# Performance work log

Hardware: AMD Instinct MI355X
Metric: run time of the kernel (lower is better)

The kernel has to match this reference:

```python
import jax, jax.numpy as jnp
import numpy as np

T, S, B, E, H = 1024, 1024, 4, 1024, 16
D = E // H
SCALE = D ** -0.5


def setup_inputs() -> dict:
    key = jax.random.key(0)
    ks = jax.random.split(key, 10)
    std = 0.02
    return {
        "q": jax.random.normal(ks[0], (T, B, E), jnp.float32),
        "k": jax.random.normal(ks[1], (S, B, E), jnp.float32),
        "v": jax.random.normal(ks[2], (S, B, E), jnp.float32),
        "Wq": jax.random.normal(ks[3], (E, E), jnp.float32) * std,
        "Wk": jax.random.normal(ks[4], (E, E), jnp.float32) * std,
        "Wv": jax.random.normal(ks[5], (E, E), jnp.float32) * std,
        "Wp": jax.random.normal(ks[6], (E, E), jnp.float32) * std,
        "bp": jnp.zeros((E,), jnp.float32),
        "attn_bias": jax.random.normal(ks[7], (B, H, T, S), jnp.float32) * std,
        "key_padding_mask": jax.random.bernoulli(ks[8], 0.1, (B, S)),
    }


def reference(q, k, v, Wq, Wk, Wv, Wp, bp, attn_bias, key_padding_mask):
    # projections (no bias: qkv_bias=False); torch Linear is x @ W.T
    qh = (q @ Wq.T).reshape(T, B, H, D).transpose(1, 2, 0, 3) * SCALE  # [B,H,T,D]
    kh = (k @ Wk.T).reshape(S, B, H, D).transpose(1, 2, 0, 3)          # [B,H,S,D]
    vh = (v @ Wv.T).reshape(S, B, H, D).transpose(1, 2, 0, 3)          # [B,H,S,D]

    scores = jnp.einsum("bhid,bhjd->bhij", qh, kh) + attn_bias        # [B,H,T,S]
    # detached max-subtract (as in original)
    scores = scores - jax.lax.stop_gradient(scores.max(axis=-1, keepdims=True))

    mask = key_padding_mask[:, None, None, :]                          # [B,1,1,S], True = masked
    neg = jnp.finfo(scores.dtype).min
    attn = jax.nn.softmax(jnp.where(mask, neg, scores), axis=-1)
    attn = jnp.where(mask, jnp.zeros((), scores.dtype), attn)          # XSoftmax: zero masked probs

    out = jnp.einsum("bhij,bhjd->bhid", attn, vh)                      # [B,H,T,D]
    out = out.transpose(2, 0, 1, 3).reshape(T, B, E)                   # [T,B,E]
    out = out @ Wp.T + bp                                              # output projection
    return (out, attn)
```

## Files before the change

kernel.cpp:

```cpp
#include <hip/hip_runtime.h>
#include <math.h>

constexpr int T_ = 1024, S_ = 1024, B_ = 4, E_ = 1024, H_ = 16, D_ = 64;
constexpr float SCALE_ = 0.125f;
constexpr size_t NH_ = (size_t)B_ * H_ * T_ * D_;
constexpr size_t EE_ = (size_t)E_ * E_;

typedef _Float16 h8 __attribute__((ext_vector_type(8)));
typedef _Float16 h4 __attribute__((ext_vector_type(4)));
typedef float f4 __attribute__((ext_vector_type(4)));

__device__ inline f4 mfma16(h8 a, h8 b, f4 c) {
    return __builtin_amdgcn_mfma_f32_16x16x32_f16(a, b, c, 0, 0, 0);
}

__device__ inline void gload_lds16(const void* g, void* l) {
    __builtin_amdgcn_global_load_lds(
        (const __attribute__((address_space(1))) void*)g,
        (__attribute__((address_space(3))) void*)l, 16, 0, 0);
}

__global__ __launch_bounds__(256) void cvt_all(
    const float* __restrict__ q, const float* __restrict__ k,
    const float* __restrict__ v, const float* __restrict__ wq,
    const float* __restrict__ wk, const float* __restrict__ wv,
    const float* __restrict__ wp, _Float16* __restrict__ dst)
{
    const int i8 = blockIdx.x * 256 + threadIdx.x;
    constexpr int BIG = (int)(NH_ / 8);
    constexpr int WSZ = (int)(EE_ / 8);
    const float* src;
    int loc;
    if (i8 < 3 * BIG) {
        int t = i8 / BIG; loc = i8 - t * BIG;
        src = t == 0 ? q : (t == 1 ? k : v);
    } else {
        int r = i8 - 3 * BIG;
        int t = r / WSZ; loc = r - t * WSZ;
        src = t == 0 ? wq : (t == 1 ? wk : (t == 2 ? wv : wp));
    }
    const float* p = src + (size_t)loc * 8;
    float4 a = *(const float4*)p;
    float4 b = *(const float4*)(p + 4);
    h8 o;
    o[0] = (_Float16)a.x; o[1] = (_Float16)a.y;
    o[2] = (_Float16)a.z; o[3] = (_Float16)a.w;
    o[4] = (_Float16)b.x; o[5] = (_Float16)b.y;
    o[6] = (_Float16)b.z; o[7] = (_Float16)b.w;
    *(h8*)&dst[(size_t)i8 * 8] = o;
}

template <typename EPI>
__device__ inline void gemm_core(
    const _Float16* __restrict__ A, const _Float16* __restrict__ W,
    int m0, int n0, EPI epi)
{
    __shared__ _Float16 As[64][64];
    __shared__ _Float16 Bs[128][64];

    const int tid = threadIdx.x;
    const int w = tid >> 6, l = tid & 63, lr = l & 15, lg = l >> 4;
    const int wr = w >> 2, wc = w & 3;

    const int srow = (w << 3) + (l >> 3);
    const int sg   = (l & 7) ^ (srow & 7);
    char* AsB = (char*)As;
    char* BsB = (char*)Bs;
    char* ldsA  = AsB + w * 1024;
    char* ldsB0 = BsB + w * 1024;
    char* ldsB1 = BsB + 8192 + w * 1024;

    f4 acc[2][2];
#pragma unroll
    for (int mi = 0; mi < 2; ++mi)
#pragma unroll
        for (int ni = 0; ni < 2; ++ni) acc[mi][ni] = (f4){0.f, 0.f, 0.f, 0.f};

    for (int k0 = 0; k0 < 1024; k0 += 64) {
        gload_lds16(&A[(size_t)(m0 + srow) * 1024 + k0 + sg * 8], ldsA);
        gload_lds16(&W[(size_t)(n0 + srow) * 1024 + k0 + sg * 8], ldsB0);
        gload_lds16(&W[(size_t)(n0 + 64 + srow) * 1024 + k0 + sg * 8], ldsB1);
        __syncthreads();
#pragma unroll
        for (int kk = 0; kk < 2; ++kk) {
            h8 af[2], bf[2];
#pragma unroll
            for (int mi = 0; mi < 2; ++mi) {
                int r = wr * 32 + mi * 16 + lr, kc = kk * 4 + lg;
                af[mi] = *(const h8*)(AsB + r * 128 + ((kc ^ (r & 7)) << 4));
            }
#pragma unroll
            for (int ni = 0; ni < 2; ++ni) {
                int r = wc * 32 + ni * 16 + lr, kc = kk * 4 + lg;
                bf[ni] = *(const h8*)(BsB + r * 128 + ((kc ^ (r & 7)) << 4));
            }
#pragma unroll
            for (int mi = 0; mi < 2; ++mi)
#pragma unroll
                for (int ni = 0; ni < 2; ++ni)
                    acc[mi][ni] = mfma16(af[mi], bf[ni], acc[mi][ni]);
        }
        __syncthreads();
    }

#pragma unroll
    for (int mi = 0; mi < 2; ++mi)
#pragma unroll
        for (int ni = 0; ni < 2; ++ni)
#pragma unroll
            for (int r = 0; r < 4; ++r) {
                int row = m0 + wr * 32 + mi * 16 + lg * 4 + r;
                int col = n0 + wc * 32 + ni * 16 + lr;
                epi(row, col, acc[mi][ni][r]);
            }
}

template <typename EPI>
__device__ inline void gemm_core128(
    const _Float16* __restrict__ A, const _Float16* __restrict__ W,
    int m0, int n0, EPI epi)
{
    __shared__ _Float16 As[128][64];
    __shared__ _Float16 Bs[128][64];

    const int tid = threadIdx.x;
    const int w = tid >> 6, l = tid & 63, lr = l & 15, lg = l >> 4;
    const int wr = w >> 2, wc = w & 3;

    char* AsB = (char*)As;
    char* BsB = (char*)Bs;

    f4 acc[4][2];
#pragma unroll
    for (int mi = 0; mi < 4; ++mi)
#pragma unroll
        for (int ni = 0; ni < 2; ++ni) acc[mi][ni] = (f4){0.f, 0.f, 0.f, 0.f};

    for (int k0 = 0; k0 < 1024; k0 += 64) {
#pragma unroll
        for (int d = 0; d < 2; ++d) {
            int row = w * 16 + d * 8 + (l >> 3);
            int sg = (l & 7) ^ (row & 7);
            gload_lds16(&A[(size_t)(m0 + row) * 1024 + k0 + sg * 8],
                        AsB + (w * 16 + d * 8) * 128);
            gload_lds16(&W[(size_t)(n0 + row) * 1024 + k0 + sg * 8],
                        BsB + (w * 16 + d * 8) * 128);
        }
        __syncthreads();
#pragma unroll
        for (int kk = 0; kk < 2; ++kk) {
            h8 af[4], bf[2];
#pragma unroll
            for (int mi = 0; mi < 4; ++mi) {
                int r = wr * 64 + mi * 16 + lr, kc = kk * 4 + lg;
                af[mi] = *(const h8*)(AsB + r * 128 + ((kc ^ (r & 7)) << 4));
            }
#pragma unroll
            for (int ni = 0; ni < 2; ++ni) {
                int r = wc * 32 + ni * 16 + lr, kc = kk * 4 + lg;
                bf[ni] = *(const h8*)(BsB + r * 128 + ((kc ^ (r & 7)) << 4));
            }
#pragma unroll
            for (int mi = 0; mi < 4; ++mi)
#pragma unroll
                for (int ni = 0; ni < 2; ++ni)
                    acc[mi][ni] = mfma16(af[mi], bf[ni], acc[mi][ni]);
        }
        __syncthreads();
    }

#pragma unroll
    for (int mi = 0; mi < 4; ++mi)
#pragma unroll
        for (int ni = 0; ni < 2; ++ni)
#pragma unroll
            for (int r = 0; r < 4; ++r) {
                int row = m0 + wr * 64 + mi * 16 + lg * 4 + r;
                int col = n0 + wc * 32 + ni * 16 + lr;
                epi(row, col, acc[mi][ni][r]);
            }
}

__global__ __launch_bounds__(512) void qkv_gemm(
    const _Float16* __restrict__ q16, const _Float16* __restrict__ k16,
    const _Float16* __restrict__ v16, const _Float16* __restrict__ Wq16,
    const _Float16* __restrict__ Wk16, const _Float16* __restrict__ Wv16,
    _Float16* __restrict__ qh, _Float16* __restrict__ kh,
    _Float16* __restrict__ vhT)
{
    const int z = blockIdx.z;
    const _Float16* A = z == 0 ? q16 : (z == 1 ? k16 : v16);
    const _Float16* W = z == 0 ? Wq16 : (z == 1 ? Wk16 : Wv16);
    _Float16* C = z == 0 ? qh : (z == 1 ? kh : vhT);
    const float scale = (z == 0) ? SCALE_ : 1.0f;
    const int m0 = blockIdx.x * 128, n0 = blockIdx.y * 128;

    if (z < 2) {
        gemm_core128(A, W, m0, n0, [&](int row, int col, float vv) {
            int t = row >> 2, b = row & 3, h = col >> 6, d = col & 63;
            C[(((size_t)b * H_ + h) * T_ + t) * D_ + d] = (_Float16)(vv * scale);
        });
    } else {
        gemm_core128(A, W, m0, n0, [&](int row, int col, float vv) {
            int s = row >> 2, b = row & 3, h = col >> 6, d = col & 63;
            C[(((size_t)b * H_ + h) * D_ + d) * S_ + s] = (_Float16)vv;
        });
    }
}

__global__ __launch_bounds__(512) void out_gemm(
    const _Float16* __restrict__ oh, const _Float16* __restrict__ Wp16,
    const float* __restrict__ bp, float* __restrict__ out)
{
    const int m0 = blockIdx.x * 64, n0 = blockIdx.y * 128;
    gemm_core(oh, Wp16, m0, n0, [&](int row, int col, float vv) {
        out[(size_t)row * E_ + col] = vv + bp[col];
    });
}

__global__ __launch_bounds__(512, 6) void fused_attn(
    const _Float16* __restrict__ qh, const _Float16* __restrict__ kh,
    const _Float16* __restrict__ vhT, const float* __restrict__ bias,
    const int* __restrict__ mask, float* __restrict__ attn,
    _Float16* __restrict__ oh)
{
    __shared__ _Float16 Pf[16 * 1024];
    __shared__ int aux_i[1024];
    __shared__ float wsum[8][16];
    __shared__ float sinv16[16];
    char* Pb = (char*)Pf;

    const int bid = blockIdx.x;
    const int vid = (bid & 7) * 512 + (bid >> 3);
    const int bh = vid >> 6;
    const int t0 = (vid & 63) * 16;
    const int b = bh >> 4, h = bh & 15;
    const int tid = threadIdx.x;
    const int w = tid >> 6, l = tid & 63, lr = l & 15, lg = l >> 4;

    const float* bbase = bias + ((size_t)bh * T_ + t0) * S_;
    const int brow_ = l >> 2, bq_ = l & 3;
    f4 bv[8];
#pragma unroll
    for (int j = 0; j < 8; ++j)
        bv[j] = *(const f4*)&bbase[(size_t)brow_ * S_ + w * 128 + j * 16 + bq_ * 4];

    const _Float16* qbase = qh + ((size_t)bh * T_ + t0) * D_;
    h8 qf0 = *(const h8*)&qbase[(size_t)lr * D_ + lg * 8];
    h8 qf1 = *(const h8*)&qbase[(size_t)lr * D_ + 32 + lg * 8];
    __builtin_amdgcn_sched_barrier(0);

    for (int i = tid; i < S_; i += 512) aux_i[i] = mask[(size_t)b * S_ + i];
    __syncthreads();

    const _Float16* kbase = kh + (size_t)bh * S_ * D_;
    const int wbase = w * 128;
    const int srcLane = lr * 4 + lg;

    float rs = 0.f;
#pragma unroll
    for (int sub = 0; sub < 8; ++sub) {
        int s0 = wbase + sub * 16;
        h8 kf0 = *(const h8*)&kbase[(size_t)(s0 + lr) * D_ + lg * 8];
        h8 kf1 = *(const h8*)&kbase[(size_t)(s0 + lr) * D_ + 32 + lg * 8];
        f4 c = (f4){0.f, 0.f, 0.f, 0.f};
        c = mfma16(kf0, qf0, c);
        c = mfma16(kf1, qf1, c);
        float b0 = __shfl(bv[sub][0], srcLane);
        float b1 = __shfl(bv[sub][1], srcLane);
        float b2 = __shfl(bv[sub][2], srcLane);
        float b3 = __shfl(bv[sub][3], srcLane);
        int4 mv = *(const int4*)&aux_i[s0 + lg * 4];
        float p0 = mv.x ? 0.f : __expf(c[0] + b0);
        float p1 = mv.y ? 0.f : __expf(c[1] + b1);
        float p2 = mv.z ? 0.f : __expf(c[2] + b2);
        float p3 = mv.w ? 0.f : __expf(c[3] + b3);
        rs += (p0 + p1) + (p2 + p3);
        h4 pv;
        pv[0] = (_Float16)p0; pv[1] = (_Float16)p1;
        pv[2] = (_Float16)p2; pv[3] = (_Float16)p3;
        int off = (lr * 2048 + (s0 + lg * 4) * 2) ^ ((lr & 7) << 4);
        *(h4*)(Pb + off) = pv;
    }
    rs += __shfl_xor(rs, 16); rs += __shfl_xor(rs, 32);
    if (l < 16) wsum[w][lr] = rs;
    __syncthreads();

    {
        const int rr2 = tid >> 5;
        const int c2  = tid & 31;
        float s8 = 0.f;
#pragma unroll
        for (int ww = 0; ww < 8; ++ww) s8 += wsum[ww][rr2];
        float inv = 1.0f / s8;
        if (c2 == 0) sinv16[rr2] = inv;
        float* arow = attn + ((size_t)bh * T_ + t0 + rr2) * S_;
#pragma unroll
        for (int j = 0; j < 8; ++j) {
            int col = c2 * 4 + j * 128;
            int off = (rr2 * 2048 + col * 2) ^ ((rr2 & 7) << 4);
            h4 p = *(const h4*)(Pb + off);
            f4 o = {(float)p[0] * inv, (float)p[1] * inv,
                    (float)p[2] * inv, (float)p[3] * inv};
            __builtin_nontemporal_store(o, (f4*)&arow[col]);
        }
    }

    {
        const int sh = w & 1, dbase = (w >> 1) * 16;
        const _Float16* vbase = vhT + (size_t)bh * D_ * S_;
        f4 acc = (f4){0.f, 0.f, 0.f, 0.f};
#pragma unroll 8
        for (int kc = 0; kc < 16; ++kc) {
            int s0 = sh * 512 + kc * 32;
            int off = (lr * 2048 + (s0 + lg * 8) * 2) ^ ((lr & 7) << 4);
            h8 pf = *(const h8*)(Pb + off);
            h8 vf = *(const h8*)&vbase[(size_t)(dbase + lr) * S_ + s0 + lg * 8];
            acc = mfma16(pf, vf, acc);
        }
        float* pvred = (float*)aux_i;
        if (sh) {
#pragma unroll
            for (int r = 0; r < 4; ++r)
                pvred[(lg * 4 + r) * 64 + dbase + lr] = acc[r];
        }
        __syncthreads();
        if (!sh) {
#pragma unroll
            for (int r = 0; r < 4; ++r) {
                int t = lg * 4 + r;
                float o = (acc[r] + pvred[t * 64 + dbase + lr]) * sinv16[t];
                oh[((size_t)(t0 + t) * B_ + b) * E_ + h * 64 + dbase + lr] = (_Float16)o;
            }
        }
    }
}

extern "C" void kernel_launch(void* const* d_in, const int* in_sizes, int n_in,
                              void* d_out, int out_size, void* d_ws, size_t ws_size,
                              hipStream_t stream)
{
    const float* q    = (const float*)d_in[0];
    const float* k    = (const float*)d_in[1];
    const float* v    = (const float*)d_in[2];
    const float* Wq   = (const float*)d_in[3];
    const float* Wk   = (const float*)d_in[4];
    const float* Wv   = (const float*)d_in[5];
    const float* Wp   = (const float*)d_in[6];
    const float* bp   = (const float*)d_in[7];
    const float* bias = (const float*)d_in[8];
    const int*   mask = (const int*)d_in[9];

    float* out  = (float*)d_out;
    float* attn = out + (size_t)T_ * B_ * E_;

    _Float16* qh   = (_Float16*)d_ws;
    _Float16* kh   = qh + NH_;
    _Float16* vhT  = kh + NH_;
    _Float16* oh   = vhT + NH_;
    _Float16* q16  = oh + NH_;
    _Float16* k16  = q16 + NH_;
    _Float16* v16  = k16 + NH_;
    _Float16* Wq16 = v16 + NH_;
    _Float16* Wk16 = Wq16 + EE_;
    _Float16* Wv16 = Wk16 + EE_;
    _Float16* Wp16 = Wv16 + EE_;

    dim3 blk(512);

    cvt_all<<<dim3(8192), dim3(256), 0, stream>>>(q, k, v, Wq, Wk, Wv, Wp, q16);

    qkv_gemm<<<dim3(32, 8, 3), blk, 0, stream>>>(
        q16, k16, v16, Wq16, Wk16, Wv16, qh, kh, vhT);

    fused_attn<<<dim3(4096), blk, 0, stream>>>(qh, kh, vhT, bias, mask, attn, oh);

    out_gemm<<<dim3(64, 8), blk, 0, stream>>>(oh, Wp16, bp, out);
}
```

Baseline: 256.9 us.

## Process two query tiles per attention block with software-prefetched bias and Q

Each fused attention block now handles two 16-row query tiles instead of one, halving the grid. While the first tile is computed, the bias rows and Q fragments for the second tile are prefetched into registers. The mask is read directly from global memory instead of being staged in LDS. The register budget is raised by lowering launch-bounds occupancy from 6 to 4 blocks, which may reduce latency hiding across blocks.

New measurement: 268.7 us. 4.6% more time.

```diff
diff --git a/kernel.cpp b/kernel.cpp
--- a/kernel.cpp
+++ b/kernel.cpp
@@ -218,122 +218,140 @@
     });
 }
 
-__global__ __launch_bounds__(512, 6) void fused_attn(
+__global__ __launch_bounds__(512, 4) void fused_attn(
     const _Float16* __restrict__ qh, const _Float16* __restrict__ kh,
     const _Float16* __restrict__ vhT, const float* __restrict__ bias,
     const int* __restrict__ mask, float* __restrict__ attn,
     _Float16* __restrict__ oh)
 {
     __shared__ _Float16 Pf[16 * 1024];
-    __shared__ int aux_i[1024];
+    __shared__ float pvred[1024];
     __shared__ float wsum[8][16];
     __shared__ float sinv16[16];
     char* Pb = (char*)Pf;
 
     const int bid = blockIdx.x;
-    const int vid = (bid & 7) * 512 + (bid >> 3);
-    const int bh = vid >> 6;
-    const int t0 = (vid & 63) * 16;
+    const int vid = (bid & 7) * 256 + (bid >> 3);
+    const int bh = vid >> 5;
+    const int tbase = (vid & 31) * 32;
     const int b = bh >> 4, h = bh & 15;
     const int tid = threadIdx.x;
     const int w = tid >> 6, l = tid & 63, lr = l & 15, lg = l >> 4;
-
-    const float* bbase = bias + ((size_t)bh * T_ + t0) * S_;
-    const int brow_ = l >> 2, bq_ = l & 3;
-    f4 bv[8];
-#pragma unroll
-    for (int j = 0; j < 8; ++j)
-        bv[j] = *(const f4*)&bbase[(size_t)brow_ * S_ + w * 128 + j * 16 + bq_ * 4];
-
-    const _Float16* qbase = qh + ((size_t)bh * T_ + t0) * D_;
-    h8 qf0 = *(const h8*)&qbase[(size_t)lr * D_ + lg * 8];
-    h8 qf1 = *(const h8*)&qbase[(size_t)lr * D_ + 32 + lg * 8];
-    __builtin_amdgcn_sched_barrier(0);
-
-    for (int i = tid; i < S_; i += 512) aux_i[i] = mask[(size_t)b * S_ + i];
-    __syncthreads();
-
-    const _Float16* kbase = kh + (size_t)bh * S_ * D_;
     const int wbase = w * 128;
     const int srcLane = lr * 4 + lg;
 
-    float rs = 0.f;
-#pragma unroll
-    for (int sub = 0; sub < 8; ++sub) {
-        int s0 = wbase + sub * 16;
-        h8 kf0 = *(const h8*)&kbase[(size_t)(s0 + lr) * D_ + lg * 8];
-        h8 kf1 = *(const h8*)&kbase[(size_t)(s0 + lr) * D_ + 32 + lg * 8];
-        f4 c = (f4){0.f, 0.f, 0.f, 0.f};
-        c = mfma16(kf0, qf0, c);
-        c = mfma16(kf1, qf1, c);
-        float b0 = __shfl(bv[sub][0], srcLane);
-        float b1 = __shfl(bv[sub][1], srcLane);
-        float b2 = __shfl(bv[sub][2], srcLane);
-        float b3 = __shfl(bv[sub][3], srcLane);
-        int4 mv = *(const int4*)&aux_i[s0 + lg * 4];
-        float p0 = mv.x ? 0.f : __expf(c[0] + b0);
-        float p1 = mv.y ? 0.f : __expf(c[1] + b1);
-        float p2 = mv.z ? 0.f : __expf(c[2] + b2);
-        float p3 = mv.w ? 0.f : __expf(c[3] + b3);
-        rs += (p0 + p1) + (p2 + p3);
-        h4 pv;
-        pv[0] = (_Float16)p0; pv[1] = (_Float16)p1;
-        pv[2] = (_Float16)p2; pv[3] = (_Float16)p3;
-        int off = (lr * 2048 + (s0 + lg * 4) * 2) ^ ((lr & 7) << 4);
-        *(h4*)(Pb + off) = pv;
-    }
-    rs += __shfl_xor(rs, 16); rs += __shfl_xor(rs, 32);
-    if (l < 16) wsum[w][lr] = rs;
-    __syncthreads();
-
+    const _Float16* kbase = kh + (size_t)bh * S_ * D_;
+    const _Float16* vbase = vhT + (size_t)bh * D_ * S_;
+    const int* mrow = mask + (size_t)b * S_ + wbase + lg * 4;
+    const int brow_ = l >> 2, bq_ = l & 3;
+
+    f4 bv0[8];
     {
-        const int rr2 = tid >> 5;
-        const int c2  = tid & 31;
-        float s8 = 0.f;
-#pragma unroll
-        for (int ww = 0; ww < 8; ++ww) s8 += wsum[ww][rr2];
-        float inv = 1.0f / s8;
-        if (c2 == 0) sinv16[rr2] = inv;
-        float* arow = attn + ((size_t)bh * T_ + t0 + rr2) * S_;
-#pragma unroll
-        for (int j = 0; j < 8; ++j) {
-            int col = c2 * 4 + j * 128;
-            int off = (rr2 * 2048 + col * 2) ^ ((rr2 & 7) << 4);
-            h4 p = *(const h4*)(Pb + off);
-            f4 o = {(float)p[0] * inv, (float)p[1] * inv,
-                    (float)p[2] * inv, (float)p[3] * inv};
-            __builtin_nontemporal_store(o, (f4*)&arow[col]);
-        }
-    }
-
-    {
-        const int sh = w & 1, dbase = (w >> 1) * 16;
-        const _Float16* vbase = vhT + (size_t)bh * D_ * S_;
-        f4 acc = (f4){0.f, 0.f, 0.f, 0.f};
+        const float* bb = bias + ((size_t)bh * T_ + tbase) * S_;
+#pragma unroll
+        for (int j = 0; j < 8; ++j)
+            bv0[j] = *(const f4*)&bb[(size_t)brow_ * S_ + wbase + j * 16 + bq_ * 4];
+    }
+    const _Float16* qb0 = qh + ((size_t)bh * T_ + tbase) * D_;
+    h8 q0a = *(const h8*)&qb0[(size_t)lr * D_ + lg * 8];
+    h8 q0b = *(const h8*)&qb0[(size_t)lr * D_ + 32 + lg * 8];
+
+    f4 bv1[8];
+    h8 q1a, q1b;
+
+    auto tile = [&](int t0, f4 (&bv)[8], h8 qfa, h8 qfb,
+                    bool pre, f4 (&bvN)[8], h8& qNa, h8& qNb) {
+        if (pre) {
+            const float* bb = bias + ((size_t)bh * T_ + t0 + 16) * S_;
+#pragma unroll
+            for (int j = 0; j < 8; ++j)
+                bvN[j] = *(const f4*)&bb[(size_t)brow_ * S_ + wbase + j * 16 + bq_ * 4];
+            const _Float16* qbN = qh + ((size_t)bh * T_ + t0 + 16) * D_;
+            qNa = *(const h8*)&qbN[(size_t)lr * D_ + lg * 8];
+            qNb = *(const h8*)&qbN[(size_t)lr * D_ + 32 + lg * 8];
+        }
+
+        float rs = 0.f;
+#pragma unroll
+        for (int sub = 0; sub < 8; ++sub) {
+            int s0 = wbase + sub * 16;
+            h8 kf0 = *(const h8*)&kbase[(size_t)(s0 + lr) * D_ + lg * 8];
+            h8 kf1 = *(const h8*)&kbase[(size_t)(s0 + lr) * D_ + 32 + lg * 8];
+            f4 c = (f4){0.f, 0.f, 0.f, 0.f};
+            c = mfma16(kf0, qfa, c);
+            c = mfma16(kf1, qfb, c);
+            float b0 = __shfl(bv[sub][0], srcLane);
+            float b1 = __shfl(bv[sub][1], srcLane);
+            float b2 = __shfl(bv[sub][2], srcLane);
+            float b3 = __shfl(bv[sub][3], srcLane);
+            int4 mv = *(const int4*)&mrow[sub * 16];
+            float p0 = mv.x ? 0.f : __expf(c[0] + b0);
+            float p1 = mv.y ? 0.f : __expf(c[1] + b1);
+            float p2 = mv.z ? 0.f : __expf(c[2] + b2);
+            float p3 = mv.w ? 0.f : __expf(c[3] + b3);
+            rs += (p0 + p1) + (p2 + p3);
+            h4 pv;
+            pv[0] = (_Float16)p0; pv[1] = (_Float16)p1;
+            pv[2] = (_Float16)p2; pv[3] = (_Float16)p3;
+            int off = (lr * 2048 + (s0 + lg * 4) * 2) ^ ((lr & 7) << 4);
+            *(h4*)(Pb + off) = pv;
+        }
+        rs += __shfl_xor(rs, 16); rs += __shfl_xor(rs, 32);
+        if (l < 16) wsum[w][lr] = rs;
+        __syncthreads();
+
+        {
+            const int rr2 = tid >> 5;
+            const int c2  = tid & 31;
+            float s8 = 0.f;
+#pragma unroll
+            for (int ww = 0; ww < 8; ++ww) s8 += wsum[ww][rr2];
+            float inv = 1.0f / s8;
+            if (c2 == 0) sinv16[rr2] = inv;
+            float* arow = attn + ((size_t)bh * T_ + t0 + rr2) * S_;
+#pragma unroll
+            for (int j = 0; j < 8; ++j) {
+                int col = c2 * 4 + j * 128;
+                int off = (rr2 * 2048 + col * 2) ^ ((rr2 & 7) << 4);
+                h4 p = *(const h4*)(Pb + off);
+                f4 o = {(float)p[0] * inv, (float)p[1] * inv,
+                        (float)p[2] * inv, (float)p[3] * inv};
+                __builtin_nontemporal_store(o, (f4*)&arow[col]);
+            }
+        }
+
+        {
+            const int sh = w & 1, dbase = (w >> 1) * 16;
+            f4 acc = (f4){0.f, 0.f, 0.f, 0.f};
 #pragma unroll 8
-        for (int kc = 0; kc < 16; ++kc) {
-            int s0 = sh * 512 + kc * 32;
-            int off = (lr * 2048 + (s0 + lg * 8) * 2) ^ ((lr & 7) << 4);
-            h8 pf = *(const h8*)(Pb + off);
-            h8 vf = *(const h8*)&vbase[(size_t)(dbase + lr) * S_ + s0 + lg * 8];
-            acc = mfma16(pf, vf, acc);
-        }
-        float* pvred = (float*)aux_i;
-        if (sh) {
-#pragma unroll
-            for (int r = 0; r < 4; ++r)
-                pvred[(lg * 4 + r) * 64 + dbase + lr] = acc[r];
-        }
-        __syncthreads();
-        if (!sh) {
-#pragma unroll
-            for (int r = 0; r < 4; ++r) {
-                int t = lg * 4 + r;
-                float o = (acc[r] + pvred[t * 64 + dbase + lr]) * sinv16[t];
-                oh[((size_t)(t0 + t) * B_ + b) * E_ + h * 64 + dbase + lr] = (_Float16)o;
-            }
-        }
-    }
+            for (int kc = 0; kc < 16; ++kc) {
+                int s0 = sh * 512 + kc * 32;
+                int off = (lr * 2048 + (s0 + lg * 8) * 2) ^ ((lr & 7) << 4);
+                h8 pf = *(const h8*)(Pb + off);
+                h8 vf = *(const h8*)&vbase[(size_t)(dbase + lr) * S_ + s0 + lg * 8];
+                acc = mfma16(pf, vf, acc);
+            }
+            if (sh) {
+#pragma unroll
+                for (int r = 0; r < 4; ++r)
+                    pvred[(lg * 4 + r) * 64 + dbase + lr] = acc[r];
+            }
+            __syncthreads();
+            if (!sh) {
+#pragma unroll
+                for (int r = 0; r < 4; ++r) {
+                    int t = lg * 4 + r;
+                    float o = (acc[r] + pvred[t * 64 + dbase + lr]) * sinv16[t];
+                    oh[((size_t)(t0 + t) * B_ + b) * E_ + h * 64 + dbase + lr] =
+                        (_Float16)o;
+                }
+            }
+        }
+        __syncthreads();
+    };
+
+    tile(tbase,      bv0, q0a, q0b, true,  bv1, q1a, q1b);
+    tile(tbase + 16, bv1, q1a, q1b, false, bv0, q0a, q0b);
 }
 
 extern "C" void kernel_launch(void* const* d_in, const int* in_sizes, int n_in,
@@ -373,7 +391,7 @@
     qkv_gemm<<<dim3(32, 8, 3), blk, 0, stream>>>(
         q16, k16, v16, Wq16, Wk16, Wv16, qh, kh, vhT);
 
-    fused_attn<<<dim3(4096), blk, 0, stream>>>(qh, kh, vhT, bias, mask, attn, oh);
+    fused_attn<<<dim3(2048), blk, 0, stream>>>(qh, kh, vhT, bias, mask, attn, oh);
 
     out_gemm<<<dim3(64, 8), blk, 0, stream>>>(oh, Wp16, bp, out);
 }
```
